# Kernel tuning notes

Hardware: AMD Instinct MI355X
Metric: run time of the kernel (lower is better)

## Reference

```python
import jax, jax.numpy as jnp
import numpy as np
from jax import lax

DIM = 96
B, H, W = 4, 256, 256


def setup_inputs() -> dict:
    key = jax.random.key(0)
    ks = jax.random.split(key, 20)
    f = lambda k, s, scale=0.05: (jax.random.normal(k, s, dtype=jnp.float32) * scale)
    d = DIM
    return {
        "x": jax.random.normal(ks[0], (B, d, H, W), dtype=jnp.float32),
        "prompt": jax.random.normal(ks[1], (B, d), dtype=jnp.float32),
        "scale_weights": jax.random.uniform(ks[2], (B, 3), dtype=jnp.float32),
        "ln_w": jnp.ones((d,), jnp.float32),
        "ln_b": jnp.zeros((d,), jnp.float32),
        "e0_pw_w": f(ks[3], (d, d)),       # expert0 pointwise 1x1: [out, in]
        "e0_pw_b": f(ks[4], (d,)),
        "e0_dw_w": f(ks[5], (d, 1, 3, 3)),  # depthwise 3x3
        "e0_dw_b": f(ks[6], (d,)),
        "e1_dw_w": f(ks[7], (d, 1, 3, 3)),  # depthwise 3x3, dilation 2
        "e1_dw_b": f(ks[8], (d,)),
        "e2_dw_w": f(ks[9], (d, 1, 5, 5)),  # depthwise 5x5, dilation 3
        "e2_dw_b": f(ks[10], (d,)),
        "proj_w": f(ks[11], (d, d)),
        "proj_b": f(ks[12], (d,)),
        "ffn1_w": f(ks[13], (2 * d, d)),
        "ffn1_b": f(ks[14], (2 * d,)),
        "ffn2_w": f(ks[15], (d, 2 * d)),
        "ffn2_b": f(ks[16], (d,)),
    }


def _conv1x1(x, w, b):
    # x: [B,C,H,W], w: [O,C]
    return jnp.einsum('bchw,oc->bohw', x, w) + b[None, :, None, None]


def _dwconv(x, w, b, dilation, pad):
    # depthwise conv, w: [C,1,k,k]
    c = x.shape[1]
    y = lax.conv_general_dilated(
        x, w, window_strides=(1, 1),
        padding=[(pad, pad), (pad, pad)],
        rhs_dilation=(dilation, dilation),
        feature_group_count=c,
        dimension_numbers=('NCHW', 'OIHW', 'NCHW'))
    return y + b[None, :, None, None]


def _layernorm_c(x, w, b, eps=1e-6):
    # LayerNorm over channel dim of NCHW (torch permutes to NHWC, norms last dim)
    mu = jnp.mean(x, axis=1, keepdims=True)
    var = jnp.mean((x - mu) ** 2, axis=1, keepdims=True)
    xn = (x - mu) * lax.rsqrt(var + eps)
    return xn * w[None, :, None, None] + b[None, :, None, None]


def reference(x, prompt, scale_weights, ln_w, ln_b,
              e0_pw_w, e0_pw_b, e0_dw_w, e0_dw_b,
              e1_dw_w, e1_dw_b, e2_dw_w, e2_dw_b,
              proj_w, proj_b, ffn1_w, ffn1_b, ffn2_w, ffn2_b):
    shortcut = x
    xn = _layernorm_c(x, ln_w, ln_b)

    # Three receptive-field experts (all run densely, soft-weighted)
    e0 = _dwconv(_conv1x1(xn, e0_pw_w, e0_pw_b), e0_dw_w, e0_dw_b, dilation=1, pad=1)
    e1 = _dwconv(xn, e1_dw_w, e1_dw_b, dilation=2, pad=2)
    e2 = _dwconv(xn, e2_dw_w, e2_dw_b, dilation=3, pad=6)

    w = scale_weights  # [B,3]
    x_adaptive = (w[:, 0, None, None, None] * e0
                  + w[:, 1, None, None, None] * e1
                  + w[:, 2, None, None, None] * e2)
    x_adaptive = x_adaptive * (1.0 + prompt[:, :, None, None])

    x1 = shortcut + _conv1x1(x_adaptive, proj_w, proj_b)
    h = jax.nn.gelu(_conv1x1(x1, ffn1_w, ffn1_b), approximate=False)
    out = x1 + _conv1x1(h, ffn2_w, ffn2_b)
    return out
```

## Files before the change

kernel.cpp:

```cpp
#include <hip/hip_runtime.h>
#include <hip/hip_bf16.h>

typedef __hip_bfloat16 bf16;
typedef __attribute__((ext_vector_type(8))) __bf16 bf16x8;
typedef __attribute__((ext_vector_type(4))) float  f32x4;

#define HW   65536
#define WID  256
#define CC   96
#define NB   4
static const size_t S_ELEMS = (size_t)NB * CC * HW;

__device__ __forceinline__ float lo2f(unsigned u) { unsigned x = u << 16;        return __builtin_bit_cast(float, x); }
__device__ __forceinline__ float hi2f(unsigned u) { unsigned x = u & 0xffff0000u; return __builtin_bit_cast(float, x); }
__device__ __forceinline__ unsigned short f2bu(float f) {
    return __builtin_bit_cast(unsigned short, __float2bfloat16(f));
}

__device__ __forceinline__ float gelu_erf(float v) {
    float z  = fabsf(v) * 0.70710678118654752f;
    float t  = __builtin_amdgcn_rcpf(1.f + 0.3275911f * z);
    float poly = t * (0.254829592f + t * (-0.284496736f + t * (1.421413741f
               + t * (-1.453152027f + t * 1.061405429f))));
    float erfz = 1.f - poly * __expf(-z * z);
    float erfv = copysignf(erfz, v);
    return 0.5f * v * (1.f + erfv);
}

__global__ __launch_bounds__(256) void ln_kernel(
    const float* __restrict__ x, const float* __restrict__ lw,
    const float* __restrict__ lb, bf16* __restrict__ y)
{
    int t  = blockIdx.x * 256 + threadIdx.x;
    int b  = t >> 15;
    int hw = (t & 32767) * 2;
    size_t base = (size_t)b * CC * HW + hw;

    float s0 = 0.f, s1 = 0.f, q0 = 0.f, q1 = 0.f;
    for (int c = 0; c < CC; ++c) {
        float2 v = *reinterpret_cast<const float2*>(&x[base + (size_t)c * HW]);
        s0 += v.x; s1 += v.y; q0 += v.x * v.x; q1 += v.y * v.y;
    }
    float mu0 = s0 * (1.f / 96.f), mu1 = s1 * (1.f / 96.f);
    float rs0 = rsqrtf(q0 * (1.f / 96.f) - mu0 * mu0 + 1e-6f);
    float rs1 = rsqrtf(q1 * (1.f / 96.f) - mu1 * mu1 + 1e-6f);

    for (int c = 0; c < CC; ++c) {
        float2 v = *reinterpret_cast<const float2*>(&x[base + (size_t)c * HW]);
        float g = lw[c], be = lb[c];
        bf16 o[2];
        o[0] = __float2bfloat16((v.x - mu0) * rs0 * g + be);
        o[1] = __float2bfloat16((v.y - mu1) * rs1 * g + be);
        *reinterpret_cast<uint*>(&y[base + (size_t)c * HW]) = *reinterpret_cast<uint*>(o);
    }
}

__device__ __forceinline__ int swzo(int row, int col, int width) {
    return (row * width + col) ^ ((((row & 7) ^ ((row >> 3) & 7)) << 3));
}

template <typename TI, typename TOT, int CIN, int COUT, bool GELU, bool HASRES>
__global__ __launch_bounds__(256) void conv1x1_mfma(
    const TI* __restrict__ in, const float* __restrict__ wgt,
    const float* __restrict__ bias, const float* __restrict__ resid,
    TOT* __restrict__ out)
{
    constexpr int KSPLIT = CIN / 96;
    constexpr int OSPLIT = COUT / 96;
    constexpr int MT     = 6;
    static_assert(CIN == KSPLIT * 96 && COUT == OSPLIT * 96, "96-multiples only");

    __shared__ unsigned short s_w[96 * 96];
    __shared__ unsigned short s_x[128 * 96];
    __shared__ float          s_b[COUT];

    const int tid  = threadIdx.x;
    const int lane = tid & 63;
    const int wave = tid >> 6;
    const int q    = lane >> 4;
    const int n    = lane & 15;

    const int pos0 = blockIdx.x * 128;
    const int b    = pos0 >> 16;
    const int hw0  = pos0 & 65535;

    for (int k = tid; k < COUT; k += 256) s_b[k] = bias[k];

    const TI* inb = in + (size_t)b * CIN * HW;
    const int pl0 = wave * 32 + n;
    const int pl1 = pl0 + 16;

#pragma unroll
    for (int os = 0; os < OSPLIT; ++os) {
        f32x4 acc[MT][2];
#pragma unroll
        for (int mt = 0; mt < MT; ++mt) {
            acc[mt][0] = {0.f, 0.f, 0.f, 0.f};
            acc[mt][1] = {0.f, 0.f, 0.f, 0.f};
        }

#pragma unroll
        for (int ks = 0; ks < KSPLIT; ++ks) {
            for (int k = tid; k < 96 * 24; k += 256) {
                int o = k / 24, c4 = (k - o * 24) * 4;
                float4 w4 = *reinterpret_cast<const float4*>(
                    &wgt[(size_t)(os * 96 + o) * CIN + ks * 96 + c4]);
                ushort4 pk = make_ushort4(f2bu(w4.x), f2bu(w4.y), f2bu(w4.z), f2bu(w4.w));
                *reinterpret_cast<ushort4*>(&s_w[swzo(o, c4, 96)]) = pk;
            }
            if (KSPLIT > 1 || os == 0) {
                for (int idx = tid; idx < 48 * 16; idx += 256) {
                    const int cp = idx >> 4;
                    const int pb = idx & 15;
                    const TI* gp = inb + (size_t)(ks * 96 + 2 * cp) * HW + hw0 + pb * 8;
                    unsigned short ua[8], ub[8];
                    if constexpr (__is_same(TI, float)) {
                        float4 a0 = *reinterpret_cast<const float4*>(gp);
                        float4 a1 = *reinterpret_cast<const float4*>(gp + 4);
                        float4 b0 = *reinterpret_cast<const float4*>(gp + HW);
                        float4 b1 = *reinterpret_cast<const float4*>(gp + HW + 4);
                        ua[0]=f2bu(a0.x); ua[1]=f2bu(a0.y); ua[2]=f2bu(a0.z); ua[3]=f2bu(a0.w);
                        ua[4]=f2bu(a1.x); ua[5]=f2bu(a1.y); ua[6]=f2bu(a1.z); ua[7]=f2bu(a1.w);
                        ub[0]=f2bu(b0.x); ub[1]=f2bu(b0.y); ub[2]=f2bu(b0.z); ub[3]=f2bu(b0.w);
                        ub[4]=f2bu(b1.x); ub[5]=f2bu(b1.y); ub[6]=f2bu(b1.z); ub[7]=f2bu(b1.w);
                    } else {
                        *reinterpret_cast<uint4*>(ua) = *reinterpret_cast<const uint4*>(gp);
                        *reinterpret_cast<uint4*>(ub) = *reinterpret_cast<const uint4*>(gp + HW);
                    }
#pragma unroll
                    for (int i = 0; i < 8; ++i) {
                        uint d = (uint)ua[i] | ((uint)ub[i] << 16);
                        *reinterpret_cast<uint*>(&s_x[swzo(pb * 8 + i, 2 * cp, 96)]) = d;
                    }
                }
            }
            __syncthreads();

#pragma unroll
            for (int kt = 0; kt < 3; ++kt) {
                const int col = kt * 32 + q * 8;
                union { unsigned short u[8]; bf16x8 v; } bf0, bf1;
                *reinterpret_cast<uint4*>(bf0.u) =
                    *reinterpret_cast<const uint4*>(&s_x[swzo(pl0, col, 96)]);
                *reinterpret_cast<uint4*>(bf1.u) =
                    *reinterpret_cast<const uint4*>(&s_x[swzo(pl1, col, 96)]);
#pragma unroll
                for (int mt = 0; mt < MT; ++mt) {
                    union { unsigned short u[8]; bf16x8 v; } fa;
                    *reinterpret_cast<uint4*>(fa.u) =
                        *reinterpret_cast<const uint4*>(&s_w[swzo(mt * 16 + n, col, 96)]);
                    acc[mt][0] = __builtin_amdgcn_mfma_f32_16x16x32_bf16(fa.v, bf0.v, acc[mt][0], 0, 0, 0);
                    acc[mt][1] = __builtin_amdgcn_mfma_f32_16x16x32_bf16(fa.v, bf1.v, acc[mt][1], 0, 0, 0);
                }
            }
            if (os + 1 < OSPLIT || ks + 1 < KSPLIT)
                __syncthreads();
        }

        const int p0 = hw0 + pl0;
        const int p1 = hw0 + pl1;
        const size_t obase = (size_t)b * COUT * HW;
#pragma unroll
        for (int mt = 0; mt < MT; ++mt) {
#pragma unroll
            for (int nt = 0; nt < 2; ++nt) {
                const int p = (nt == 0) ? p0 : p1;
#pragma unroll
                for (int r = 0; r < 4; ++r) {
                    const int o = os * 96 + mt * 16 + q * 4 + r;
                    float v = acc[mt][nt][r] + s_b[o];
                    if constexpr (GELU) v = gelu_erf(v);
                    const size_t idx = obase + (size_t)o * HW + p;
                    if constexpr (HASRES) v += resid[idx];
                    if constexpr (__is_same(TOT, float)) out[idx] = v;
                    else                                 out[idx] = __float2bfloat16(v);
                }
            }
        }
    }
}

#define XR     20
#define XPITCH 22
#define TPITCH 10
#define XCOLS  268
#define TCOLS  258

__global__ __launch_bounds__(256) void experts_kernel(
    const bf16* __restrict__ xn, const bf16* __restrict__ t0,
    const float* __restrict__ w0, const float* __restrict__ b0,
    const float* __restrict__ w1, const float* __restrict__ b1,
    const float* __restrict__ w2, const float* __restrict__ b2,
    const float* __restrict__ sw, const float* __restrict__ prompt,
    bf16* __restrict__ xa)
{
    __shared__ alignas(16) unsigned short sxT[XCOLS * XPITCH];
    __shared__ alignas(16) unsigned short stT[TCOLS * TPITCH];

    const int tid  = threadIdx.x;
    const int lane = tid & 63;
    const int wave = tid >> 6;
    const int bid = blockIdx.x;
    const int h0  = (bid & 31) * 8;
    const int bc  = bid >> 5;
    const int b   = bc / 96;
    const int c   = bc - b * 96;
    const size_t pbase = (size_t)bc * HW;

    const bf16* xp = xn + pbase;
    const bf16* tp = t0 + pbase;
    uint* sx32 = reinterpret_cast<uint*>(sxT);
    uint* st32 = reinterpret_cast<uint*>(stT);

    if (tid < 132) {
        int cc = tid / 11, d = tid - cc * 11;
        int col = (cc < 6) ? cc : 256 + cc;
        sx32[col * 11 + d] = 0u;
    } else if (tid < 142) {
        int i = tid - 132;
        int col = (i < 5) ? 0 : 257;
        int d   = (i < 5) ? i : i - 5;
        st32[col * 5 + d] = 0u;
    }

    {
        const int rp = (lane >> 2) & 7;
        const int ch = 8 * wave + (lane & 3) + ((lane >> 5) << 2);
        const int gh0 = h0 - 6 + 2 * rp, gh1 = gh0 + 1;
        union { uint4 q; unsigned short u[8]; } a, bb;
        a.q  = ((unsigned)gh0 < 256u) ? *reinterpret_cast<const uint4*>(xp + gh0 * WID + ch * 8)
                                      : make_uint4(0u, 0u, 0u, 0u);
        bb.q = ((unsigned)gh1 < 256u) ? *reinterpret_cast<const uint4*>(xp + gh1 * WID + ch * 8)
                                      : make_uint4(0u, 0u, 0u, 0u);
        const int base = 11 * (6 + 8 * ch) + rp;
#pragma unroll
        for (int j = 0; j < 8; ++j)
            sx32[base + 11 * j] = (uint)a.u[j] | ((uint)bb.u[j] << 16);
    }
    if (wave == 2) {
        const int rp = 8 + ((lane >> 2) & 1);
        const int ch = (lane & 3) + (((lane >> 3) & 7) << 2);
        const int gh0 = h0 - 6 + 2 * rp, gh1 = gh0 + 1;
        union { uint4 q; unsigned short u[8]; } a, bb;
        a.q  = ((unsigned)gh0 < 256u) ? *reinterpret_cast<const uint4*>(xp + gh0 * WID + ch * 8)
                                      : make_uint4(0u, 0u, 0u, 0u);
        bb.q = ((unsigned)gh1 < 256u) ? *reinterpret_cast<const uint4*>(xp + gh1 * WID + ch * 8)
                                      : make_uint4(0u, 0u, 0u, 0u);
        const int base = 11 * (6 + 8 * ch) + rp;
#pragma unroll
        for (int j = 0; j < 8; ++j)
            sx32[base + 11 * j] = (uint)a.u[j] | ((uint)bb.u[j] << 16);
    }
    if (wave < 2) {
        const int rp = (lane >> 3) & 3;
        const int ch = 16 * wave + (lane & 7) + ((lane >> 5) << 3);
        const int gh0 = h0 - 1 + 2 * rp, gh1 = gh0 + 1;
        union { uint4 q; unsigned short u[8]; } a, bb;
        a.q  = ((unsigned)gh0 < 256u) ? *reinterpret_cast<const uint4*>(tp + gh0 * WID + ch * 8)
                                      : make_uint4(0u, 0u, 0u, 0u);
        bb.q = ((unsigned)gh1 < 256u) ? *reinterpret_cast<const uint4*>(tp + gh1 * WID + ch * 8)
                                      : make_uint4(0u, 0u, 0u, 0u);
        const int base = 5 * (1 + 8 * ch) + rp;
#pragma unroll
        for (int j = 0; j < 8; ++j)
            st32[base + 5 * j] = (uint)a.u[j] | ((uint)bb.u[j] << 16);
    }
    if (wave == 3 && lane < 32) {
        const int rp = 4;
        const int ch = lane;
        const int gh0 = h0 - 1 + 2 * rp, gh1 = gh0 + 1;
        union { uint4 q; unsigned short u[8]; } a, bb;
        a.q  = ((unsigned)gh0 < 256u) ? *reinterpret_cast<const uint4*>(tp + gh0 * WID + ch * 8)
                                      : make_uint4(0u, 0u, 0u, 0u);
        bb.q = ((unsigned)gh1 < 256u) ? *reinterpret_cast<const uint4*>(tp + gh1 * WID + ch * 8)
                                      : make_uint4(0u, 0u, 0u, 0u);
        const int base = 5 * (1 + 8 * ch) + rp;
#pragma unroll
        for (int j = 0; j < 8; ++j)
            st32[base + 5 * j] = (uint)a.u[j] | ((uint)bb.u[j] << 16);
    }

    float wk0[9], wk1[9], wk2[25];
#pragma unroll
    for (int i = 0; i < 9; ++i)  wk0[i] = w0[c * 9 + i];
#pragma unroll
    for (int i = 0; i < 9; ++i)  wk1[i] = w1[c * 9 + i];
#pragma unroll
    for (int i = 0; i < 25; ++i) wk2[i] = w2[c * 25 + i];
    const float bb0 = b0[c], bb1 = b1[c], bb2 = b2[c];
    const float s0 = sw[b * 3 + 0], s1 = sw[b * 3 + 1], s2 = sw[b * 3 + 2];
    const float pr = 1.f + prompt[b * 96 + c];

    __syncthreads();

    const int w = tid;
    float acc0[8], acc1[8], acc2[8];
#pragma unroll
    for (int r = 0; r < 8; ++r) { acc0[r] = bb0; acc1[r] = bb1; acc2[r] = bb2; }

    const unsigned short* bx = &sxT[w * XPITCH];
    const unsigned short* bt = &stT[w * TPITCH];

#pragma unroll
    for (int kw = 0; kw < 5; ++kw) {
        float cv[20];
#pragma unroll
        for (int j = 0; j < 10; ++j) {
            unsigned u = *reinterpret_cast<const unsigned*>(&bx[kw * 3 * XPITCH + 2 * j]);
            cv[2 * j]     = lo2f(u);
            cv[2 * j + 1] = hi2f(u);
        }
#pragma unroll
        for (int kh = 0; kh < 5; ++kh) {
            const float wv = wk2[kh * 5 + kw];
#pragma unroll
            for (int r = 0; r < 8; ++r) acc2[r] += wv * cv[r + 3 * kh];
        }
        if (kw == 2) {
#pragma unroll
            for (int kh = 0; kh < 3; ++kh) {
                const float wv = wk1[kh * 3 + 1];
#pragma unroll
                for (int r = 0; r < 8; ++r) acc1[r] += wv * cv[r + 2 * kh + 4];
            }
        }
    }
#pragma unroll
    for (int kwh = 0; kwh < 2; ++kwh) {
        const int kw = kwh * 2;
        float cv[12];
#pragma unroll
        for (int j = 0; j < 6; ++j) {
            unsigned u = *reinterpret_cast<const unsigned*>(&bx[(4 + 2 * kw) * XPITCH + 4 + 2 * j]);
            cv[2 * j]     = lo2f(u);
            cv[2 * j + 1] = hi2f(u);
        }
#pragma unroll
        for (int kh = 0; kh < 3; ++kh) {
            const float wv = wk1[kh * 3 + kw];
#pragma unroll
            for (int r = 0; r < 8; ++r) acc1[r] += wv * cv[r + 2 * kh];
        }
    }
#pragma unroll
    for (int kw = 0; kw < 3; ++kw) {
        float cv[10];
#pragma unroll
        for (int j = 0; j < 5; ++j) {
            unsigned u = *reinterpret_cast<const unsigned*>(&bt[kw * TPITCH + 2 * j]);
            cv[2 * j]     = lo2f(u);
            cv[2 * j + 1] = hi2f(u);
        }
#pragma unroll
        for (int kh = 0; kh < 3; ++kh) {
            const float wv = wk0[kh * 3 + kw];
#pragma unroll
            for (int r = 0; r < 8; ++r) acc0[r] += wv * cv[r + kh];
        }
    }

    bf16* op = xa + pbase + (size_t)h0 * WID + w;
#pragma unroll
    for (int r = 0; r < 8; ++r) {
        float v = (s0 * acc0[r] + s1 * acc1[r] + s2 * acc2[r]) * pr;
        op[r * WID] = __float2bfloat16(v);
    }
}

extern "C" void kernel_launch(void* const* d_in, const int* in_sizes, int n_in,
                              void* d_out, int out_size, void* d_ws, size_t ws_size,
                              hipStream_t stream)
{
    const float* x       = (const float*)d_in[0];
    const float* prompt  = (const float*)d_in[1];
    const float* sw      = (const float*)d_in[2];
    const float* ln_w    = (const float*)d_in[3];
    const float* ln_b    = (const float*)d_in[4];
    const float* e0_pw_w = (const float*)d_in[5];
    const float* e0_pw_b = (const float*)d_in[6];
    const float* e0_dw_w = (const float*)d_in[7];
    const float* e0_dw_b = (const float*)d_in[8];
    const float* e1_dw_w = (const float*)d_in[9];
    const float* e1_dw_b = (const float*)d_in[10];
    const float* e2_dw_w = (const float*)d_in[11];
    const float* e2_dw_b = (const float*)d_in[12];
    const float* proj_w  = (const float*)d_in[13];
    const float* proj_b  = (const float*)d_in[14];
    const float* ffn1_w  = (const float*)d_in[15];
    const float* ffn1_b  = (const float*)d_in[16];
    const float* ffn2_w  = (const float*)d_in[17];
    const float* ffn2_b  = (const float*)d_in[18];

    float* out = (float*)d_out;
    bf16*  ws  = (bf16*)d_ws;
    bf16*  A   = ws;
    bf16*  Bt  = ws + S_ELEMS;
    bf16*  Cx  = ws + 2 * S_ELEMS;
    bf16*  E   = ws;

    ln_kernel<<<512, 256, 0, stream>>>(x, ln_w, ln_b, A);
    conv1x1_mfma<bf16, bf16, 96, 96, false, false>
        <<<2048, 256, 0, stream>>>(A, e0_pw_w, e0_pw_b, nullptr, Bt);
    experts_kernel<<<12288, 256, 0, stream>>>(A, Bt, e0_dw_w, e0_dw_b, e1_dw_w, e1_dw_b,
                                              e2_dw_w, e2_dw_b, sw, prompt, Cx);
    conv1x1_mfma<bf16, float, 96, 96, false, true>
        <<<2048, 256, 0, stream>>>(Cx, proj_w, proj_b, x, out);
    conv1x1_mfma<float, bf16, 96, 192, true, false>
        <<<2048, 256, 0, stream>>>(out, ffn1_w, ffn1_b, nullptr, E);
    conv1x1_mfma<bf16, float, 192, 96, false, true>
        <<<2048, 256, 0, stream>>>(E, ffn2_w, ffn2_b, out, out);
}
```

Measured before the change: 484.7 us.

## Fuse projection, FFN1 with GELU, and FFN2 into one MFMA kernel

Replaces three separate 1x1-conv MFMA launches (proj plus residual, ffn1 plus GELU, ffn2 plus residual) with one kernel. Each 128-pixel tile keeps x1 and the hidden activations in shared memory as bf16, and weights are staged chunk by chunk in 96x96 pieces. This removes the global round trips of the fp32 x1 and the bf16 hidden tensor, plus two launches. In exchange it adds many __syncthreads between the weight-staging phases, stages weights repeatedly per block, and uses heavy register and LDS footprint that may lower occupancy.

```diff
diff --git a/kernel.cpp b/kernel.cpp
--- a/kernel.cpp
+++ b/kernel.cpp
@@ -178,6 +178,202 @@
             }
         }
     }
+}
+
+__global__ __launch_bounds__(256) void ffn_fused(
+    const bf16* __restrict__ xa, const float* __restrict__ x,
+    const float* __restrict__ pw, const float* __restrict__ pb,
+    const float* __restrict__ w1, const float* __restrict__ b1,
+    const float* __restrict__ w2, const float* __restrict__ b2,
+    float* __restrict__ out)
+{
+    constexpr int HP = 104;
+    __shared__ unsigned short s_w[96 * 96];
+    __shared__ unsigned short s_x1[128 * HP];
+    __shared__ unsigned short s_hx[128 * HP];
+    __shared__ float          s_bias[384];
+
+    const int tid  = threadIdx.x;
+    const int lane = tid & 63;
+    const int wave = tid >> 6;
+    const int q    = lane >> 4;
+    const int n    = lane & 15;
+
+    const int pos0 = blockIdx.x * 128;
+    const int b    = pos0 >> 16;
+    const int hw0  = pos0 & 65535;
+    const int pl0  = wave * 32 + n;
+    const int pl1  = pl0 + 16;
+
+    auto stage_w = [&](const float* W, int row0, int col0, int rstride) {
+        for (int k = tid; k < 96 * 24; k += 256) {
+            int o = k / 24, c4 = (k - o * 24) * 4;
+            float4 w4 = *reinterpret_cast<const float4*>(
+                &W[(size_t)(row0 + o) * rstride + col0 + c4]);
+            ushort4 pk = make_ushort4(f2bu(w4.x), f2bu(w4.y), f2bu(w4.z), f2bu(w4.w));
+            *reinterpret_cast<ushort4*>(&s_w[swzo(o, c4, 96)]) = pk;
+        }
+    };
+    auto gemm_swz = [&](f32x4 (&acc)[6][2]) {
+#pragma unroll
+        for (int kt = 0; kt < 3; ++kt) {
+            const int col = kt * 32 + q * 8;
+            union { unsigned short u[8]; bf16x8 v; } bf0, bf1;
+            *reinterpret_cast<uint4*>(bf0.u) =
+                *reinterpret_cast<const uint4*>(&s_hx[swzo(pl0, col, 96)]);
+            *reinterpret_cast<uint4*>(bf1.u) =
+                *reinterpret_cast<const uint4*>(&s_hx[swzo(pl1, col, 96)]);
+#pragma unroll
+            for (int mt = 0; mt < 6; ++mt) {
+                union { unsigned short u[8]; bf16x8 v; } fa;
+                *reinterpret_cast<uint4*>(fa.u) =
+                    *reinterpret_cast<const uint4*>(&s_w[swzo(mt * 16 + n, col, 96)]);
+                acc[mt][0] = __builtin_amdgcn_mfma_f32_16x16x32_bf16(fa.v, bf0.v, acc[mt][0], 0, 0, 0);
+                acc[mt][1] = __builtin_amdgcn_mfma_f32_16x16x32_bf16(fa.v, bf1.v, acc[mt][1], 0, 0, 0);
+            }
+        }
+    };
+    auto gemm_lin = [&](const unsigned short* B, f32x4 (&acc)[6][2]) {
+#pragma unroll
+        for (int kt = 0; kt < 3; ++kt) {
+            const int col = kt * 32 + q * 8;
+            union { unsigned short u[8]; bf16x8 v; } bf0, bf1;
+            *reinterpret_cast<uint4*>(bf0.u) =
+                *reinterpret_cast<const uint4*>(&B[pl0 * HP + col]);
+            *reinterpret_cast<uint4*>(bf1.u) =
+                *reinterpret_cast<const uint4*>(&B[pl1 * HP + col]);
+#pragma unroll
+            for (int mt = 0; mt < 6; ++mt) {
+                union { unsigned short u[8]; bf16x8 v; } fa;
+                *reinterpret_cast<uint4*>(fa.u) =
+                    *reinterpret_cast<const uint4*>(&s_w[swzo(mt * 16 + n, col, 96)]);
+                acc[mt][0] = __builtin_amdgcn_mfma_f32_16x16x32_bf16(fa.v, bf0.v, acc[mt][0], 0, 0, 0);
+                acc[mt][1] = __builtin_amdgcn_mfma_f32_16x16x32_bf16(fa.v, bf1.v, acc[mt][1], 0, 0, 0);
+            }
+        }
+    };
+    auto st4 = [&](unsigned short* dst, int elem, float v0, float v1, float v2, float v3) {
+        union { unsigned short u[4]; uint2 d; } t;
+        t.u[0] = f2bu(v0); t.u[1] = f2bu(v1); t.u[2] = f2bu(v2); t.u[3] = f2bu(v3);
+        *reinterpret_cast<uint2*>(&dst[elem]) = t.d;
+    };
+
+    {
+        const bf16* inb = xa + (size_t)b * 96 * HW;
+        for (int idx = tid; idx < 48 * 16; idx += 256) {
+            const int cp = idx >> 4, pbk = idx & 15;
+            const bf16* gp = inb + (size_t)(2 * cp) * HW + hw0 + pbk * 8;
+            unsigned short ua[8], ub[8];
+            *reinterpret_cast<uint4*>(ua) = *reinterpret_cast<const uint4*>(gp);
+            *reinterpret_cast<uint4*>(ub) = *reinterpret_cast<const uint4*>(gp + HW);
+#pragma unroll
+            for (int i = 0; i < 8; ++i) {
+                uint d = (uint)ua[i] | ((uint)ub[i] << 16);
+                *reinterpret_cast<uint*>(&s_hx[swzo(pbk * 8 + i, 2 * cp, 96)]) = d;
+            }
+        }
+    }
+    stage_w(pw, 0, 0, 96);
+    if (tid < 96)  s_bias[tid]       = pb[tid];
+    if (tid < 192) s_bias[96 + tid]  = b1[tid];
+    if (tid < 96)  s_bias[288 + tid] = b2[tid];
+    __syncthreads();
+
+    float xr[6][2][4];
+    {
+        const size_t xbase = (size_t)b * 96 * HW;
+#pragma unroll
+        for (int mt = 0; mt < 6; ++mt)
+#pragma unroll
+            for (int nt = 0; nt < 2; ++nt) {
+                const int p = hw0 + (nt ? pl1 : pl0);
+#pragma unroll
+                for (int r = 0; r < 4; ++r)
+                    xr[mt][nt][r] = x[xbase + (size_t)(mt * 16 + q * 4 + r) * HW + p];
+            }
+    }
+    f32x4 accp[6][2];
+#pragma unroll
+    for (int mt = 0; mt < 6; ++mt) { accp[mt][0] = {0,0,0,0}; accp[mt][1] = {0,0,0,0}; }
+    gemm_swz(accp);
+
+    float x1f[6][2][4];
+#pragma unroll
+    for (int mt = 0; mt < 6; ++mt)
+#pragma unroll
+        for (int nt = 0; nt < 2; ++nt) {
+            const int p = nt ? pl1 : pl0;
+#pragma unroll
+            for (int r = 0; r < 4; ++r)
+                x1f[mt][nt][r] = accp[mt][nt][r] + s_bias[mt * 16 + q * 4 + r] + xr[mt][nt][r];
+            st4(s_x1, p * HP + mt * 16 + q * 4,
+                x1f[mt][nt][0], x1f[mt][nt][1], x1f[mt][nt][2], x1f[mt][nt][3]);
+        }
+    __syncthreads();
+
+    stage_w(w1, 0, 0, 96);
+    __syncthreads();
+    f32x4 acc1[6][2];
+#pragma unroll
+    for (int mt = 0; mt < 6; ++mt) { acc1[mt][0] = {0,0,0,0}; acc1[mt][1] = {0,0,0,0}; }
+    gemm_lin(s_x1, acc1);
+#pragma unroll
+    for (int mt = 0; mt < 6; ++mt)
+#pragma unroll
+        for (int nt = 0; nt < 2; ++nt) {
+            const int p = nt ? pl1 : pl0;
+            float v0 = gelu_erf(acc1[mt][nt][0] + s_bias[96 + mt * 16 + q * 4 + 0]);
+            float v1 = gelu_erf(acc1[mt][nt][1] + s_bias[96 + mt * 16 + q * 4 + 1]);
+            float v2 = gelu_erf(acc1[mt][nt][2] + s_bias[96 + mt * 16 + q * 4 + 2]);
+            float v3 = gelu_erf(acc1[mt][nt][3] + s_bias[96 + mt * 16 + q * 4 + 3]);
+            st4(s_hx, p * HP + mt * 16 + q * 4, v0, v1, v2, v3);
+        }
+    __syncthreads();
+
+    stage_w(w1, 96, 0, 96);
+    __syncthreads();
+    f32x4 acc1b[6][2];
+#pragma unroll
+    for (int mt = 0; mt < 6; ++mt) { acc1b[mt][0] = {0,0,0,0}; acc1b[mt][1] = {0,0,0,0}; }
+    gemm_lin(s_x1, acc1b);
+    __syncthreads();
+
+    stage_w(w2, 0, 0, 192);
+    __syncthreads();
+    f32x4 acc2[6][2];
+#pragma unroll
+    for (int mt = 0; mt < 6; ++mt) { acc2[mt][0] = {0,0,0,0}; acc2[mt][1] = {0,0,0,0}; }
+    gemm_lin(s_hx, acc2);
+    __syncthreads();
+
+    stage_w(w2, 0, 96, 192);
+#pragma unroll
+    for (int mt = 0; mt < 6; ++mt)
+#pragma unroll
+        for (int nt = 0; nt < 2; ++nt) {
+            const int p = nt ? pl1 : pl0;
+            float v0 = gelu_erf(acc1b[mt][nt][0] + s_bias[192 + mt * 16 + q * 4 + 0]);
+            float v1 = gelu_erf(acc1b[mt][nt][1] + s_bias[192 + mt * 16 + q * 4 + 1]);
+            float v2 = gelu_erf(acc1b[mt][nt][2] + s_bias[192 + mt * 16 + q * 4 + 2]);
+            float v3 = gelu_erf(acc1b[mt][nt][3] + s_bias[192 + mt * 16 + q * 4 + 3]);
+            st4(s_hx, p * HP + mt * 16 + q * 4, v0, v1, v2, v3);
+        }
+    __syncthreads();
+    gemm_lin(s_hx, acc2);
+
+    const size_t obase = (size_t)b * 96 * HW;
+#pragma unroll
+    for (int mt = 0; mt < 6; ++mt)
+#pragma unroll
+        for (int nt = 0; nt < 2; ++nt) {
+            const int p = hw0 + (nt ? pl1 : pl0);
+#pragma unroll
+            for (int r = 0; r < 4; ++r) {
+                const int o = mt * 16 + q * 4 + r;
+                out[obase + (size_t)o * HW + p] =
+                    x1f[mt][nt][r] + acc2[mt][nt][r] + s_bias[288 + o];
+            }
+        }
 }
 
 #define XR     20
@@ -396,17 +592,12 @@
     bf16*  A   = ws;
     bf16*  Bt  = ws + S_ELEMS;
     bf16*  Cx  = ws + 2 * S_ELEMS;
-    bf16*  E   = ws;
 
     ln_kernel<<<512, 256, 0, stream>>>(x, ln_w, ln_b, A);
     conv1x1_mfma<bf16, bf16, 96, 96, false, false>
         <<<2048, 256, 0, stream>>>(A, e0_pw_w, e0_pw_b, nullptr, Bt);
     experts_kernel<<<12288, 256, 0, stream>>>(A, Bt, e0_dw_w, e0_dw_b, e1_dw_w, e1_dw_b,
                                               e2_dw_w, e2_dw_b, sw, prompt, Cx);
-    conv1x1_mfma<bf16, float, 96, 96, false, true>
-        <<<2048, 256, 0, stream>>>(Cx, proj_w, proj_b, x, out);
-    conv1x1_mfma<float, bf16, 96, 192, true, false>
-        <<<2048, 256, 0, stream>>>(out, ffn1_w, ffn1_b, nullptr, E);
-    conv1x1_mfma<bf16, float, 192, 96, false, true>
-        <<<2048, 256, 0, stream>>>(E, ffn2_w, ffn2_b, out, out);
-}
+    ffn_fused<<<2048, 256, 0, stream>>>(Cx, x, proj_w, proj_b,
+                                        ffn1_w, ffn1_b, ffn2_w, ffn2_b, out);
+}
```

Measured after the change: 495.4 us. 1.02x slower.
